# Kernel tuning notes

Measured on AMD Instinct MI355X. Metric: run time of the kernel, lower is better.

The kernel has to match this reference:

```python
import jax, jax.numpy as jnp
import numpy as np

N, K, CARD = 8192, 64, 64
LAMBDA = 0.1
BIG = 1e9  # stand-in for +inf that stays finite under fp32


def setup_inputs() -> dict:
    key = jax.random.key(0)
    k1, k2, k3, k4, k5, k6 = jax.random.split(key, 6)
    adj = jax.random.uniform(k1, (N, N), dtype=jnp.float32)
    adj = 0.5 * (adj + adj.T)  # symmetric weighted adjacency
    soft_label = jax.nn.softmax(jax.random.normal(k2, (N, K), dtype=jnp.float32), axis=-1)

    def mk_dgm(k):
        # ground-truth persistence diagram: (card, 2) with birth <= death in [0,1]
        return jnp.sort(jax.random.uniform(k, (CARD, 2), dtype=jnp.float32), axis=-1)

    return {
        "adj": adj,
        "soft_label": soft_label,
        "dgm_gt_b0": mk_dgm(k3),
        "dgm_gt_b1": mk_dgm(k4),
        "dgm_gt_n0": mk_dgm(k5),
        "dgm_gt_n1": mk_dgm(k6),
    }


def community_distance(adj, S):
    # build_community_graph: C = S^T A S (KxK community graph), turn weights
    # into a sublevel filtration distance D = 1 - C/max(C) (weight-rank style).
    C = S.T @ (adj @ S)                      # [K,K]
    C = 0.5 * (C + C.T)
    C = C / (jnp.max(C) + 1e-12)
    D = 1.0 - C
    Kn = D.shape[0]
    return D.at[jnp.diag_indices(Kn)].set(0.0)


def prim_mst(D):
    # Prim's MST over the complete K-node graph; differentiable w.r.t. D via
    # gathered edge weights (argmin indices are piecewise-constant).
    Kn = D.shape[0]
    in_tree0 = jnp.zeros(Kn, dtype=bool).at[0].set(True)

    def step(in_tree, _):
        masked = jnp.where(in_tree[:, None] & (~in_tree)[None, :], D, BIG)
        idx = jnp.argmin(masked)
        u, v = idx // Kn, idx % Kn
        return in_tree.at[v].set(True), (D[u, v], u, v)

    _, (ws, us, vs) = jax.lax.scan(step, in_tree0, None, length=Kn - 1)
    return ws, us, vs


def dgm_dim0(ws):
    # dim-0 pairs: every vertex born at 0, dies at the MST edge merging it.
    # keep_essential_parts=False drops the infinite bar. Pad/sort to CARD.
    pad = CARD - ws.shape[0]
    deaths = jax.lax.top_k(jnp.concatenate([ws, jnp.zeros(pad, ws.dtype)]), CARD)[0]
    return jnp.stack([jnp.zeros(CARD, ws.dtype), deaths], axis=-1)  # [CARD,2]


def dgm_dim1(D, us, vs):
    # dim-1 pairs of the clique (Rips) filtration: each non-MST edge (i,j)
    # births a 1-cycle at D[i,j]; its death is approximated by the cheapest
    # triangle filling it: min_k max(D[i,j], D[i,k], D[j,k]).
    Kn = D.shape[0]
    mst = jnp.zeros((Kn, Kn), dtype=bool).at[us, vs].set(True)
    mst = mst | mst.T
    # M[i,j,k] = filtration value of triangle (i,j,k)
    M = jnp.maximum(D[:, :, None], jnp.maximum(D[:, None, :], D[None, :, :]))
    kk = jnp.arange(Kn)
    bad = (kk[None, None, :] == kk[:, None, None]) | (kk[None, None, :] == kk[None, :, None])
    death = jnp.min(jnp.where(bad, BIG, M), axis=-1)     # [K,K]
    valid = jnp.triu(jnp.ones((Kn, Kn), dtype=bool), 1) & (~mst)
    pers = jnp.where(valid, death - D, -1.0)
    top_p, top_idx = jax.lax.top_k(pers.reshape(-1), CARD)
    b = jnp.take(D.reshape(-1), top_idx)
    d = jnp.take(death.reshape(-1), top_idx)
    keep = top_p > 0
    return jnp.stack([jnp.where(keep, b, 0.0), jnp.where(keep, d, 0.0)], axis=-1)


def wasserstein_w1(X, Y, eps=0.01, iters=300):
    # 1-Wasserstein diagram distance (internal_p = inf), with diagonal
    # projections as an extra sink row/column; solved by entropic Sinkhorn.
    n, m = X.shape[0], Y.shape[0]
    Cxy = jnp.max(jnp.abs(X[:, None, :] - Y[None, :, :]), axis=-1)  # [n,m]
    dX = 0.5 * (X[:, 1] - X[:, 0])  # L_inf distance to diagonal
    dY = 0.5 * (Y[:, 1] - Y[:, 0])
    C = jnp.zeros((n + 1, m + 1), X.dtype).at[:n, :m].set(Cxy).at[:n, m].set(dX).at[n, :m].set(dY)
    loga = jnp.log(jnp.concatenate([jnp.ones(n), jnp.full((1,), float(m))]))
    logb = jnp.log(jnp.concatenate([jnp.ones(m), jnp.full((1,), float(n))]))

    def step(fg, _):
        f, g = fg
        f = eps * (loga - jax.nn.logsumexp((g[None, :] - C) / eps, axis=1))
        g = eps * (logb - jax.nn.logsumexp((f[:, None] - C) / eps, axis=0))
        return (f, g), None

    (f, g), _ = jax.lax.scan(step, (jnp.zeros(n + 1), jnp.zeros(m + 1)), None, length=iters)
    P = jnp.exp((f[:, None] + g[None, :] - C) / eps)
    return jnp.sum(P * C)


def reference(adj, soft_label, dgm_gt_b0, dgm_gt_b1, dgm_gt_n0, dgm_gt_n1):
    D = community_distance(adj, soft_label)
    ws, us, vs = prim_mst(D)
    dgm0 = dgm_dim0(ws)
    dgm1 = dgm_dim1(D, us, vs)
    loss = (wasserstein_w1(dgm0, dgm_gt_b0) + wasserstein_w1(dgm1, dgm_gt_b1)
            + wasserstein_w1(dgm0, dgm_gt_n0) + wasserstein_w1(dgm1, dgm_gt_n1))
    return LAMBDA * loss
```

## Files before the change

kernel.cpp:

```cpp
#include <hip/hip_runtime.h>
#include <hip/hip_bf16.h>

#define NN 8192
#define KK 64
#define CARD 64
#define AST_OFF   0
#define CRAW_OFF  524288
#define DGM0_OFF  528384
#define DGM1_OFF  528512

__device__ __forceinline__ float rlane(float v, int l) {
  return __int_as_float(__builtin_amdgcn_readlane(__float_as_int(v), l));
}
__device__ __forceinline__ double rdlane(double x, int l) {
  int lo = __builtin_amdgcn_readlane(__double2loint(x), l);
  int hi = __builtin_amdgcn_readlane(__double2hiint(x), l);
  return __hiloint2double(hi, lo);
}

#define KSPLIT 16
#define KT 32
#define RB 256
__global__ __launch_bounds__(256, 2) void k_gemm_as(
    const float* __restrict__ A, const float* __restrict__ S,
    float* __restrict__ AST) {
  __shared__ float At[KT][RB + 1];
  __shared__ float Sl[KT][64];
  const int tid = threadIdx.x;
  const int rb = blockIdx.x >> 4;
  const int ks = blockIdx.x & 15;
  const int r0 = rb * RB;
  const int lane = tid & 63;
  const int cg = __builtin_amdgcn_readfirstlane(tid >> 6);
  const int c0 = cg * 16;

  float acc[4][16];
#pragma unroll
  for (int r = 0; r < 4; ++r)
#pragma unroll
    for (int q = 0; q < 16; ++q) acc[r][q] = 0.0f;

  const int kbeg = ks * (NN / KSPLIT);
  for (int kt = kbeg; kt < kbeg + NN / KSPLIT; kt += KT) {
#pragma unroll
    for (int p = 0; p < 8; ++p) {
      int fi = p * 256 + tid;
      int rr = fi >> 3, cc = (fi & 7) * 4;
      float4 v = *reinterpret_cast<const float4*>(
          A + (size_t)(r0 + rr) * NN + kt + cc);
      At[cc + 0][rr] = v.x; At[cc + 1][rr] = v.y;
      At[cc + 2][rr] = v.z; At[cc + 3][rr] = v.w;
    }
#pragma unroll
    for (int p = 0; p < 2; ++p) {
      int fi = p * 256 + tid;
      int rr = fi >> 4, cc = (fi & 15) * 4;
      float4 v = *reinterpret_cast<const float4*>(
          S + (size_t)(kt + rr) * KK + cc);
      *reinterpret_cast<float4*>(&Sl[rr][cc]) = v;
    }
    __syncthreads();
#pragma unroll 2
    for (int k = 0; k < KT; ++k) {
      float a0 = At[k][lane];
      float a1 = At[k][lane + 64];
      float a2 = At[k][lane + 128];
      float a3 = At[k][lane + 192];
      const float4* Sv = reinterpret_cast<const float4*>(&Sl[k][c0]);
      float4 s0 = Sv[0], s1 = Sv[1], s2 = Sv[2], s3 = Sv[3];
      float sc[16] = {s0.x, s0.y, s0.z, s0.w, s1.x, s1.y, s1.z, s1.w,
                      s2.x, s2.y, s2.z, s2.w, s3.x, s3.y, s3.z, s3.w};
#pragma unroll
      for (int q = 0; q < 16; ++q) {
        acc[0][q] = fmaf(a0, sc[q], acc[0][q]);
        acc[1][q] = fmaf(a1, sc[q], acc[1][q]);
        acc[2][q] = fmaf(a2, sc[q], acc[2][q]);
        acc[3][q] = fmaf(a3, sc[q], acc[3][q]);
      }
    }
    __syncthreads();
  }
#pragma unroll
  for (int r = 0; r < 4; ++r)
#pragma unroll
    for (int q = 0; q < 16; ++q)
      unsafeAtomicAdd(&AST[(size_t)(c0 + q) * NN + r0 + r * 64 + lane],
                      acc[r][q]);
}

__global__ __launch_bounds__(256) void k_gemm_c(
    const float* __restrict__ S, const float* __restrict__ AST,
    float* __restrict__ CRAW) {
  const int j = blockIdx.x & 63;
  const int iseg = blockIdx.x >> 6;
  const int lane = threadIdx.x & 63;
  const int s4 = __builtin_amdgcn_readfirstlane(threadIdx.x >> 6);
  const int i0 = iseg * 1024 + s4 * 256;
  const float* astj = AST + (size_t)j * NN + i0;
  float acc = 0.0f;
  for (int i = 0; i < 256; i += 4) {
    float4 a4 = *reinterpret_cast<const float4*>(astj + i);
    const float* Srow = S + (size_t)(i0 + i) * KK + lane;
    acc = fmaf(a4.x, Srow[0 * KK], acc);
    acc = fmaf(a4.y, Srow[1 * KK], acc);
    acc = fmaf(a4.z, Srow[2 * KK], acc);
    acc = fmaf(a4.w, Srow[3 * KK], acc);
  }
  __shared__ float red[4][64];
  red[s4][lane] = acc;
  __syncthreads();
  if (threadIdx.x < 64) {
    unsafeAtomicAdd(&CRAW[j * 64 + lane],
                    red[0][lane] + red[1][lane] + red[2][lane] + red[3][lane]);
  }
}

__global__ __launch_bounds__(256) void k_topo(
    const float* __restrict__ CRAW, float* __restrict__ DGM0,
    float* __restrict__ DGM1, float* __restrict__ out) {
  __shared__ float Dl[64 * 66];
  __shared__ float red[4];
  __shared__ float wsE[64];
  __shared__ int usE[64], vsE[64];
  __shared__ unsigned char msk[4096];
  __shared__ float death[4096];
  __shared__ float pers[4096];
  __shared__ float rv[4];
  __shared__ int ri[4];
  const int t = threadIdx.x;

  if (t == 0) out[0] = 0.0f;

  float lmax = -1e30f;
#pragma unroll
  for (int m = 0; m < 16; ++m) {
    int idx = t + 256 * m;
    int a = idx >> 6, b = idx & 63;
    float v = 0.5f * (CRAW[idx] + CRAW[b * 64 + a]);
    Dl[a * 66 + b] = v;
    lmax = fmaxf(lmax, v);
  }
  for (int o = 32; o > 0; o >>= 1) lmax = fmaxf(lmax, __shfl_xor(lmax, o));
  if ((t & 63) == 0) red[t >> 6] = lmax;
  __syncthreads();
  const float mx = fmaxf(fmaxf(red[0], red[1]), fmaxf(red[2], red[3]));
  const float inv = 1.0f / (mx + 1e-12f);
  __syncthreads();
#pragma unroll
  for (int m = 0; m < 16; ++m) {
    int idx = t + 256 * m;
    int a = idx >> 6, b = idx & 63;
    float v = 1.0f - Dl[a * 66 + b] * inv;
    Dl[a * 66 + b] = (a == b) ? 0.0f : v;
  }
  __syncthreads();

  if (t < 64) {
    const int lane = t;
    bool intree = (lane == 0);
    float key = Dl[0 * 66 + lane];
    int par = 0;
    for (int step = 0; step < 63; ++step) {
      float kv = intree ? 1e9f : key;
      int ki = lane;
      for (int o = 32; o > 0; o >>= 1) {
        float ov = __shfl_xor(kv, o);
        int oi = __shfl_xor(ki, o);
        if (ov < kv || (ov == kv && oi < ki)) { kv = ov; ki = oi; }
      }
      int pu = __shfl(par, ki);
      if (lane == 0) { wsE[step] = kv; usE[step] = pu; vsE[step] = ki; }
      if (lane == ki) intree = true;
      float dn = Dl[ki * 66 + lane];
      if (!intree && dn < key) { key = dn; par = ki; }
    }
  }
  __syncthreads();

  for (int idx = t; idx < 4096; idx += 256) msk[idx] = 0;
  __syncthreads();
  if (t < 63) {
    int u = usE[t], v = vsE[t];
    msk[u * 64 + v] = 1;
    msk[v * 64 + u] = 1;
  }
  __syncthreads();

  if (t < 64) {
    float wv = (t < 63) ? wsE[t] : 0.0f;
    int rank = 0;
    for (int o = 0; o < 64; ++o) {
      float wo = (o < 63) ? wsE[o] : 0.0f;
      rank += (wo > wv) || (wo == wv && o < t);
    }
    DGM0[rank * 2 + 0] = 0.0f;
    DGM0[rank * 2 + 1] = wv;
  }

  for (int p = t; p < 4096; p += 256) {
    int i = p >> 6, j = p & 63;
    float dij = Dl[i * 66 + j];
    float tmin = 1e9f;
#pragma unroll 8
    for (int k2 = 0; k2 < 64; ++k2) {
      float m2 = fmaxf(Dl[i * 66 + k2], Dl[j * 66 + k2]);
      tmin = fminf(tmin, (k2 == i || k2 == j) ? 1e9f : m2);
    }
    float de = fmaxf(dij, tmin);
    death[p] = de;
    bool valid = (j > i) && (!msk[p]);
    pers[p] = valid ? (de - dij) : -1.0f;
  }
  __syncthreads();

  for (int r = 0; r < 64; ++r) {
    float bv = -1e30f;
    int bi = 0;
    for (int p = t; p < 4096; p += 256) {
      float v = pers[p];
      if (v > bv) { bv = v; bi = p; }
    }
    for (int o = 32; o > 0; o >>= 1) {
      float ov = __shfl_xor(bv, o);
      int oi = __shfl_xor(bi, o);
      if (ov > bv || (ov == bv && oi < bi)) { bv = ov; bi = oi; }
    }
    if ((t & 63) == 0) { rv[t >> 6] = bv; ri[t >> 6] = bi; }
    __syncthreads();
    if (t == 0) {
      for (int q = 1; q < 4; ++q)
        if (rv[q] > bv || (rv[q] == bv && ri[q] < bi)) { bv = rv[q]; bi = ri[q]; }
      bool keep = bv > 0.0f;
      int i = bi >> 6, j = bi & 63;
      DGM1[r * 2 + 0] = keep ? Dl[i * 66 + j] : 0.0f;
      DGM1[r * 2 + 1] = keep ? death[bi] : 0.0f;
      pers[bi] = -3.0f;
    }
    __syncthreads();
  }
}

__global__ __launch_bounds__(512) void k_sinkhorn(
    const float* __restrict__ DGM0, const float* __restrict__ DGM1,
    const float* __restrict__ G0, const float* __restrict__ G1,
    const float* __restrict__ G2, const float* __restrict__ G3,
    float* __restrict__ out) {
  const int b = blockIdx.x;
  const float* X = (b & 1) ? DGM1 : DGM0;
  const float* Y = (b == 0) ? G0 : (b == 1) ? G1 : (b == 2) ? G2 : G3;

  __shared__ double Wd[65][66];
  __shared__ float Cf[65][66];
  __shared__ double pmu[8][66];
  __shared__ double pmv[8][66];
  __shared__ double u64s, v64s;
  __shared__ float wsum[8];

  const int t = threadIdx.x;
  const int lane = t & 63;
  const int w = __builtin_amdgcn_readfirstlane(t >> 6);
  const float INVE = 100.0f;

  for (int idx = t; idx < 65 * 65; idx += 512) {
    int i = idx / 65, j = idx - i * 65;
    float v;
    if (i < 64) {
      float xb = X[i * 2], xd = X[i * 2 + 1];
      if (j < 64)
        v = fmaxf(fabsf(xb - Y[j * 2]), fabsf(xd - Y[j * 2 + 1]));
      else
        v = 0.5f * (xd - xb);
    } else {
      v = (j < 64) ? 0.5f * (Y[j * 2 + 1] - Y[j * 2]) : 0.0f;
    }
    Cf[i][j] = v * INVE;
  }
  if (t == 0) v64s = 1.0;
  __syncthreads();
  for (int idx = t; idx < 65 * 65; idx += 512) {
    int i = idx / 65, j = idx - i * 65;
    Wd[i][j] = exp(-(double)Cf[i][j]);
  }
  __syncthreads();

  double WF[8], WG[8], WG64r[8], WC64r[8];
  float CeF[8], Ce64r[8];
#pragma unroll
  for (int q = 0; q < 8; ++q) {
    int jq = 8 * w + q;
    WF[q] = Wd[lane][jq];
    WG[q] = Wd[jq][lane];
    WG64r[q] = Wd[64][jq];
    WC64r[q] = Wd[jq][64];
    CeF[q] = Cf[lane][jq];
    Ce64r[q] = Cf[64][jq];
  }
  const double WF8 = Wd[lane][64];
  const double W64c = Wd[64][lane];
  const float CF8e = Cf[lane][64];

  double u = 1.0, v = 1.0;

  for (int it = 0; it < 300; ++it) {
    {
      double part = 0.0, r64 = 0.0;
#pragma unroll
      for (int q = 0; q < 8; ++q) {
        double sv = rdlane(v, 8 * w + q);
        part = fma(WF[q], sv, part);
        r64 = fma(WG64r[q], sv, r64);
      }
      pmu[w][lane] = part;
      if (lane == 0) pmu[w][64] = r64;
    }
    __syncthreads();
    {
      double s = pmu[0][lane];
#pragma unroll
      for (int q2 = 1; q2 < 8; ++q2) s += pmu[q2][lane];
      double v64u = v64s;
      s = fma(WF8, v64u, s);
      u = 1.0 / s;
      if (w == 0) {
        double s64 = v64u;
#pragma unroll
        for (int q2 = 0; q2 < 8; ++q2) s64 += pmu[q2][64];
        if (lane == 0) u64s = 64.0 / s64;
      }
    }
    {
      double part = 0.0, c64 = 0.0;
#pragma unroll
      for (int q = 0; q < 8; ++q) {
        double su = rdlane(u, 8 * w + q);
        part = fma(WG[q], su, part);
        c64 = fma(WC64r[q], su, c64);
      }
      pmv[w][lane] = part;
      if (lane == 0) pmv[w][64] = c64;
    }
    __syncthreads();
    {
      double s = pmv[0][lane];
#pragma unroll
      for (int q2 = 1; q2 < 8; ++q2) s += pmv[q2][lane];
      double u64u = u64s;
      s = fma(W64c, u64u, s);
      v = 1.0 / s;
      if (w == 1) {
        double s64 = u64u;
#pragma unroll
        for (int q2 = 0; q2 < 8; ++q2) s64 += pmv[q2][64];
        if (lane == 0) v64s = 64.0 / s64;
      }
    }
  }
  __syncthreads();

  const double u64u = u64s, v64u = v64s;
  double acc = 0.0, accU = 0.0;
#pragma unroll
  for (int q = 0; q < 8; ++q) {
    double sv = rdlane(v, 8 * w + q);
    acc += u * WF[q] * sv * (double)CeF[q];
    accU += WG64r[q] * sv * (double)Ce64r[q];
  }
  accU *= u64u;
  if (w == 0) acc += u * WF8 * v64u * (double)CF8e;
  float af = (float)acc;
  for (int o = 32; o > 0; o >>= 1) af += __shfl_xor(af, o);
  if (lane == 0) wsum[w] = af + (float)accU;
  __syncthreads();
  if (t == 0) {
    float tot = 0.0f;
#pragma unroll
    for (int q = 0; q < 8; ++q) tot += wsum[q];
    atomicAdd(out, 0.1f * 0.01f * tot);
  }
}

extern "C" void kernel_launch(void* const* d_in, const int* in_sizes, int n_in,
                              void* d_out, int out_size, void* d_ws,
                              size_t ws_size, hipStream_t stream) {
  const float* A = (const float*)d_in[0];
  const float* S = (const float*)d_in[1];
  const float* G0 = (const float*)d_in[2];
  const float* G1 = (const float*)d_in[3];
  const float* G2 = (const float*)d_in[4];
  const float* G3 = (const float*)d_in[5];
  float* out = (float*)d_out;
  float* ws = (float*)d_ws;

  float* AST = ws + AST_OFF;
  float* CRAW = ws + CRAW_OFF;
  float* DGM0 = ws + DGM0_OFF;
  float* DGM1 = ws + DGM1_OFF;

  (void)hipMemsetAsync(AST, 0, (size_t)(64 * NN + 64 * 64) * sizeof(float),
                       stream);

  k_gemm_as<<<dim3(32 * KSPLIT), dim3(256), 0, stream>>>(A, S, AST);
  k_gemm_c<<<dim3(64 * 8), dim3(256), 0, stream>>>(S, AST, CRAW);
  k_topo<<<dim3(1), dim3(256), 0, stream>>>(CRAW, DGM0, DGM1, out);
  k_sinkhorn<<<dim3(4), dim3(512), 0, stream>>>(DGM0, DGM1, G0, G1, G2, G3,
                                                out);
}
```

Measured before the change: 894.5 us.

## Run Sinkhorn iterations in a single wavefront without block barriers

Rewrites the Sinkhorn kernel to use one 64-lane wavefront per diagram pair instead of eight waves. Each lane keeps its full row and column of the kernel matrix in registers (128 doubles) and does the matvecs with readlane broadcasts and shuffle reductions. This removes the two __syncthreads and the LDS partial-sum exchanges in each of the 300 iterations. In exchange each lane does eight times more serial FP64 FMAs and register pressure is high, which risks spills.

```diff
diff --git a/kernel.cpp b/kernel.cpp
--- a/kernel.cpp
+++ b/kernel.cpp
@@ -240,7 +240,7 @@
   }
 }
 
-__global__ __launch_bounds__(512) void k_sinkhorn(
+__global__ __launch_bounds__(64, 1) void k_sinkhorn(
     const float* __restrict__ DGM0, const float* __restrict__ DGM1,
     const float* __restrict__ G0, const float* __restrict__ G1,
     const float* __restrict__ G2, const float* __restrict__ G3,
@@ -249,19 +249,13 @@
   const float* X = (b & 1) ? DGM1 : DGM0;
   const float* Y = (b == 0) ? G0 : (b == 1) ? G1 : (b == 2) ? G2 : G3;
 
+  __shared__ float Cf[65][66];
   __shared__ double Wd[65][66];
-  __shared__ float Cf[65][66];
-  __shared__ double pmu[8][66];
-  __shared__ double pmv[8][66];
-  __shared__ double u64s, v64s;
-  __shared__ float wsum[8];
-
-  const int t = threadIdx.x;
-  const int lane = t & 63;
-  const int w = __builtin_amdgcn_readfirstlane(t >> 6);
+
+  const int lane = threadIdx.x;
   const float INVE = 100.0f;
 
-  for (int idx = t; idx < 65 * 65; idx += 512) {
+  for (int idx = lane; idx < 65 * 65; idx += 64) {
     int i = idx / 65, j = idx - i * 65;
     float v;
     if (i < 64) {
@@ -275,108 +269,68 @@
     }
     Cf[i][j] = v * INVE;
   }
-  if (t == 0) v64s = 1.0;
-  __syncthreads();
-  for (int idx = t; idx < 65 * 65; idx += 512) {
+  __syncthreads();
+  for (int idx = lane; idx < 65 * 65; idx += 64) {
     int i = idx / 65, j = idx - i * 65;
     Wd[i][j] = exp(-(double)Cf[i][j]);
   }
   __syncthreads();
 
-  double WF[8], WG[8], WG64r[8], WC64r[8];
-  float CeF[8], Ce64r[8];
-#pragma unroll
-  for (int q = 0; q < 8; ++q) {
-    int jq = 8 * w + q;
-    WF[q] = Wd[lane][jq];
-    WG[q] = Wd[jq][lane];
-    WG64r[q] = Wd[64][jq];
-    WC64r[q] = Wd[jq][64];
-    CeF[q] = Cf[lane][jq];
-    Ce64r[q] = Cf[64][jq];
-  }
-  const double WF8 = Wd[lane][64];
-  const double W64c = Wd[64][lane];
-  const float CF8e = Cf[lane][64];
-
-  double u = 1.0, v = 1.0;
+  double WF[64], WG[64];
+#pragma unroll
+  for (int j = 0; j < 64; ++j) WF[j] = Wd[lane][j];
+#pragma unroll
+  for (int i = 0; i < 64; ++i) WG[i] = Wd[i][lane];
+  const double WF8  = Wd[lane][64];
+  const double W64r = Wd[64][lane];
+
+  double u = 1.0, v = 1.0, u64 = 1.0, v64 = 1.0;
 
   for (int it = 0; it < 300; ++it) {
-    {
-      double part = 0.0, r64 = 0.0;
-#pragma unroll
-      for (int q = 0; q < 8; ++q) {
-        double sv = rdlane(v, 8 * w + q);
-        part = fma(WF[q], sv, part);
-        r64 = fma(WG64r[q], sv, r64);
-      }
-      pmu[w][lane] = part;
-      if (lane == 0) pmu[w][64] = r64;
-    }
-    __syncthreads();
-    {
-      double s = pmu[0][lane];
-#pragma unroll
-      for (int q2 = 1; q2 < 8; ++q2) s += pmu[q2][lane];
-      double v64u = v64s;
-      s = fma(WF8, v64u, s);
-      u = 1.0 / s;
-      if (w == 0) {
-        double s64 = v64u;
-#pragma unroll
-        for (int q2 = 0; q2 < 8; ++q2) s64 += pmu[q2][64];
-        if (lane == 0) u64s = 64.0 / s64;
-      }
-    }
-    {
-      double part = 0.0, c64 = 0.0;
-#pragma unroll
-      for (int q = 0; q < 8; ++q) {
-        double su = rdlane(u, 8 * w + q);
-        part = fma(WG[q], su, part);
-        c64 = fma(WC64r[q], su, c64);
-      }
-      pmv[w][lane] = part;
-      if (lane == 0) pmv[w][64] = c64;
-    }
-    __syncthreads();
-    {
-      double s = pmv[0][lane];
-#pragma unroll
-      for (int q2 = 1; q2 < 8; ++q2) s += pmv[q2][lane];
-      double u64u = u64s;
-      s = fma(W64c, u64u, s);
-      v = 1.0 / s;
-      if (w == 1) {
-        double s64 = u64u;
-#pragma unroll
-        for (int q2 = 0; q2 < 8; ++q2) s64 += pmv[q2][64];
-        if (lane == 0) v64s = 64.0 / s64;
-      }
-    }
-  }
-  __syncthreads();
-
-  const double u64u = u64s, v64u = v64s;
-  double acc = 0.0, accU = 0.0;
-#pragma unroll
-  for (int q = 0; q < 8; ++q) {
-    double sv = rdlane(v, 8 * w + q);
-    acc += u * WF[q] * sv * (double)CeF[q];
-    accU += WG64r[q] * sv * (double)Ce64r[q];
-  }
-  accU *= u64u;
-  if (w == 0) acc += u * WF8 * v64u * (double)CF8e;
+    double t64 = W64r * v;
+#pragma unroll
+    for (int o = 32; o > 0; o >>= 1) t64 += __shfl_xor(t64, o);
+
+    double a0 = 0.0, a1 = 0.0, a2 = 0.0, a3 = 0.0;
+#pragma unroll
+    for (int j = 0; j < 64; j += 4) {
+      a0 = fma(WF[j + 0], rdlane(v, j + 0), a0);
+      a1 = fma(WF[j + 1], rdlane(v, j + 1), a1);
+      a2 = fma(WF[j + 2], rdlane(v, j + 2), a2);
+      a3 = fma(WF[j + 3], rdlane(v, j + 3), a3);
+    }
+    double s = ((a0 + a1) + (a2 + a3)) + WF8 * v64;
+    u = 1.0 / s;
+    u64 = 64.0 / (t64 + v64);
+
+    double t8 = WF8 * u;
+#pragma unroll
+    for (int o = 32; o > 0; o >>= 1) t8 += __shfl_xor(t8, o);
+
+    double b0 = 0.0, b1 = 0.0, b2 = 0.0, b3 = 0.0;
+#pragma unroll
+    for (int i = 0; i < 64; i += 4) {
+      b0 = fma(WG[i + 0], rdlane(u, i + 0), b0);
+      b1 = fma(WG[i + 1], rdlane(u, i + 1), b1);
+      b2 = fma(WG[i + 2], rdlane(u, i + 2), b2);
+      b3 = fma(WG[i + 3], rdlane(u, i + 3), b3);
+    }
+    double sv = ((b0 + b1) + (b2 + b3)) + W64r * u64;
+    v = 1.0 / sv;
+    v64 = 64.0 / (t8 + u64);
+  }
+
+  double acc = 0.0;
+#pragma unroll
+  for (int j = 0; j < 64; ++j)
+    acc += u * WF[j] * rdlane(v, j) * (double)Cf[lane][j];
+  acc += u * WF8 * v64 * (double)Cf[lane][64];
+  acc += u64 * W64r * v * (double)Cf[64][lane];
   float af = (float)acc;
+#pragma unroll
   for (int o = 32; o > 0; o >>= 1) af += __shfl_xor(af, o);
-  if (lane == 0) wsum[w] = af + (float)accU;
-  __syncthreads();
-  if (t == 0) {
-    float tot = 0.0f;
-#pragma unroll
-    for (int q = 0; q < 8; ++q) tot += wsum[q];
-    atomicAdd(out, 0.1f * 0.01f * tot);
-  }
+  if (lane == 0)
+    atomicAdd(out, 0.1f * 0.01f * af);
 }
 
 extern "C" void kernel_launch(void* const* d_in, const int* in_sizes, int n_in,
@@ -402,6 +356,6 @@
   k_gemm_as<<<dim3(32 * KSPLIT), dim3(256), 0, stream>>>(A, S, AST);
   k_gemm_c<<<dim3(64 * 8), dim3(256), 0, stream>>>(S, AST, CRAW);
   k_topo<<<dim3(1), dim3(256), 0, stream>>>(CRAW, DGM0, DGM1, out);
-  k_sinkhorn<<<dim3(4), dim3(512), 0, stream>>>(DGM0, DGM1, G0, G1, G2, G3,
-                                                out);
-}
+  k_sinkhorn<<<dim3(4), dim3(64), 0, stream>>>(DGM0, DGM1, G0, G1, G2, G3,
+                                               out);
+}
```

Measured after the change: 1.002 ms. 12.1% more time.
